# Performance work log

Hardware: AMD Instinct MI355X
Metric: run time of the kernel (lower is better)

Reference implementation:

```python
import jax, jax.numpy as jnp
import numpy as np

N, F, T, E, TS, H = 10000, 64, 8, 160000, 200, 128
K = max(1, int(N * 0.5))
EPS = 1e-8


def layer_norm(x, g, b):
    m = x.mean(-1, keepdims=True)
    v = ((x - m) ** 2).mean(-1, keepdims=True)
    return (x - m) * jax.lax.rsqrt(v + 1e-5) * g + b


def setup_inputs() -> dict:
    key = jax.random.key(0)
    ks = jax.random.split(key, 16)
    s = lambda i, shape, scale=0.05: jax.random.normal(ks[i], shape, jnp.float32) * scale
    return {
        "x_seq": jax.random.normal(ks[0], (T, N, F), jnp.float32),
        "h0": jnp.zeros((N, H), jnp.float32),
        "c0": jnp.zeros((N, H), jnp.float32),
        "time_series": jax.random.normal(ks[1], (TS, N), jnp.float32),
        "Wx": s(2, (4, H, F)),            # gate order: input, forget, output, modulation
        "bx": jnp.zeros((4, H), jnp.float32),
        "Wh": s(3, (4, H, H)),
        "bh": jnp.zeros((4, H), jnp.float32),
        "ln_mod_g": jnp.ones((H,), jnp.float32),
        "ln_mod_b": jnp.zeros((H,), jnp.float32),
        "map_W": s(4, (3, H, H)),         # p1_i0, p2_i0, p2_i1
        "pool_vec": jax.random.normal(ks[5], (H, 1), jnp.float32),
        "lstm_Wih": s(6, (4 * H, N), 0.01),
        "lstm_Whh": s(7, (4 * H, H)),
        "lstm_bih": jnp.zeros((4 * H,), jnp.float32),
        "lstm_bhh": jnp.zeros((4 * H,), jnp.float32),
        "mlp_W1": s(8, (H, 2 * H)),
        "mlp_b1": jnp.zeros((H,), jnp.float32),
        "mlp_ln_g": jnp.ones((H,), jnp.float32),
        "mlp_ln_b": jnp.zeros((H,), jnp.float32),
        "mlp_W2": s(9, (H // 2, H)),
        "mlp_b2": jnp.zeros((H // 2,), jnp.float32),
        "mlp_W3": s(10, (1, H // 2)),
        "mlp_b3": jnp.zeros((1,), jnp.float32),
        "edge_index": jax.random.randint(ks[11], (2, E), 0, N, jnp.int32),
    }


def _forward(x_seq, h0, c0, time_series, Wx, bx, Wh, bh, ln_mod_g, ln_mod_b,
             map_W, pool_vec, lstm_Wih, lstm_Whh, lstm_bih, lstm_bhh,
             mlp_W1, mlp_b1, mlp_ln_g, mlp_ln_b, mlp_W2, mlp_b2, mlp_W3, mlp_b3,
             edge_index):
    src, dst = edge_index[0], edge_index[1]
    # GCN symmetric norm with self-loops: D^{-1/2}(A+I)D^{-1/2}
    deg = 1.0 + jax.ops.segment_sum(jnp.ones((E,), jnp.float32), dst, num_segments=N)
    dis = jax.lax.rsqrt(deg)
    enorm = dis[src] * dis[dst]
    self_norm = dis * dis

    def aggregate(hfeat):  # one shared gather/scatter for all 4 gates, [N, 4H]
        out = jax.ops.segment_sum(hfeat[src] * enorm[:, None], dst, num_segments=N)
        return out + hfeat * self_norm[:, None]

    bias = (bx + bh).reshape(4 * H)

    def cell(x, h, c):
        lin = (jnp.einsum('nf,ghf->ngh', x, Wx).reshape(N, 4 * H)
               + jnp.einsum('nd,ghd->ngh', h, Wh).reshape(N, 4 * H))
        pre = (aggregate(lin) + bias).reshape(N, 4, H)  # aggregation is linear -> fuse x- and h-branches
        i = jax.nn.relu(pre[:, 0])
        f = jax.nn.relu(pre[:, 1])
        o = jax.nn.relu(pre[:, 2])
        g = jnp.tanh(layer_norm(pre[:, 3], ln_mod_g, ln_mod_b))
        c_new = f * c + i * g
        return o * jnp.tanh(c_new), c_new

    # jump_connection_parallel over strides p in {1, 2}
    last = []
    for p in (1, 2):
        for off in range(p):
            h, c = h0, c0
            for t in range(off, T, p):
                h, c = cell(x_seq[t], h, c)
            last.append(h)
    hidden = sum(last[j] @ map_W[j].T for j in range(3))  # p1_i0 + p2_i0 + p2_i1

    # DGPool
    v = pool_vec / (jnp.linalg.norm(pool_vec) + EPS)
    sc = (hidden @ v).squeeze(-1)
    sc = (sc - sc.mean()) / (sc.std() + EPS)
    sig = jax.nn.sigmoid(sc)
    x_scaled = hidden * sig[:, None]
    _, idx = jax.lax.top_k(sig, K)
    new_x = x_scaled[idx]
    ss = -jnp.sort(-sig)
    pool_loss = -(jnp.log(ss[:K] + EPS).sum() + jnp.log(1.0 - ss[K:] + EPS).sum()) / N
    high = new_x.mean(axis=0)

    # raw time-series LSTM (torch gate order i, f, g, o)
    def step(carry, x_t):
        hh, cc = carry
        z = lstm_Wih @ x_t + lstm_bih + lstm_Whh @ hh + lstm_bhh
        i_, f_, g_, o_ = jnp.split(z, 4)
        cc = jax.nn.sigmoid(f_) * cc + jax.nn.sigmoid(i_) * jnp.tanh(g_)
        return (jax.nn.sigmoid(o_) * jnp.tanh(cc), cc), None

    (h_last, _), _ = jax.lax.scan(step, (jnp.zeros(H, jnp.float32), jnp.zeros(H, jnp.float32)), time_series)

    fusion = jnp.concatenate([high, h_last])
    m = jax.nn.relu(mlp_W1 @ fusion + mlp_b1)
    m = layer_norm(m, mlp_ln_g, mlp_ln_b)      # dropout = identity (eval mode)
    m = jax.nn.relu(mlp_W2 @ m + mlp_b2)
    pred = mlp_W3 @ m + mlp_b3
    return pred, pool_loss


def reference(x_seq, h0, c0, time_series, Wx, bx, Wh, bh, ln_mod_g, ln_mod_b,
              map_W, pool_vec, lstm_Wih, lstm_Whh, lstm_bih, lstm_bhh,
              mlp_W1, mlp_b1, mlp_ln_g, mlp_ln_b, mlp_W2, mlp_b2, mlp_W3, mlp_b3,
              edge_index):
    return _forward(x_seq, h0, c0, time_series, Wx, bx, Wh, bh, ln_mod_g, ln_mod_b,
                    map_W, pool_vec, lstm_Wih, lstm_Whh, lstm_bih, lstm_bhh,
                    mlp_W1, mlp_b1, mlp_ln_g, mlp_ln_b, mlp_W2, mlp_b2, mlp_W3, mlp_b3,
                    edge_index)
```

## Files before the change

kernel.cpp:

```cpp
#include <hip/hip_runtime.h>
#include <hip/hip_bf16.h>
#include <math.h>

#define NN 10000
#define FF 64
#define TSTEPS 8
#define EE 160000
#define TSS 200
#define HH 128
#define KK 5000
#define G4 512
#define KIN 192
#define EPSF 1e-8f

typedef __attribute__((ext_vector_type(8))) short short8v;
typedef __attribute__((ext_vector_type(4))) float f32x4;

__device__ inline float wred(float v){
  #pragma unroll
  for (int off = 32; off > 0; off >>= 1) v += __shfl_xor(v, off);
  return v;
}

__device__ inline unsigned short f2b(float f) {
  union { __hip_bfloat16 h; unsigned short u; } cv;
  cv.h = __float2bfloat16(f);
  return cv.u;
}
__device__ inline float b2f(unsigned short u) {
  return __uint_as_float(((unsigned int)u) << 16);
}


__global__ void k_setup_w(const float* Wx, const float* Wh, const float* bx, const float* bh,
                          const float* mapW, unsigned short* Wfrag, float* biasC, float* mapWr) {
  int idx = blockIdx.x * 256 + threadIdx.x;
  {
    int jj = idx & 7, l = (idx >> 3) & 63, ntg = (idx >> 9) & 31, ks = idx >> 14;
    int k = ks * 32 + ((l >> 4) << 3) + jj;
    int gh = ntg * 16 + (l & 15);
    int g = gh >> 7, hh = gh & 127;
    float v = (k < FF) ? Wx[(g * HH + hh) * FF + k] : Wh[(g * HH + hh) * HH + (k - FF)];
    Wfrag[idx] = f2b(v);
  }
  if (idx < G4) biasC[idx] = bx[idx] + bh[idx];
  if (idx < 3 * HH * HH) {
    int s = idx / (HH * HH), r = idx % (HH * HH);
    int d = r / HH, j = r % HH;
    mapWr[idx] = mapW[(s * HH + j) * HH + d];
  }
}

__global__ void k_zero(int* deg, int* cursor, int* rank, float* acc, float* high) {
  int i = blockIdx.x * 256 + threadIdx.x;
  if (i < NN) { deg[i] = 0; cursor[i] = 0; rank[i] = 0; }
  if (i < 16) acc[i] = 0.f;
  if (i < 128) high[i] = 0.f;
}

__global__ void k_deg(const int* ei, int* deg) {
  int e = blockIdx.x * 256 + threadIdx.x;
  if (e < EE) atomicAdd(&deg[ei[EE + e]], 1);
}

__global__ void k_norm(const int* deg, float* dis, float* self_norm) {
  int n = blockIdx.x * 256 + threadIdx.x;
  if (n < NN) {
    float d = 1.0f + (float)deg[n];
    dis[n] = rsqrtf(d);
    self_norm[n] = 1.0f / d;
  }
}

__global__ void k_scan(const int* deg, int* row_ptr, int n) {
  __shared__ int buf[1024];
  __shared__ int carry;
  if (threadIdx.x == 0) carry = 0;
  __syncthreads();
  for (int base = 0; base < n; base += 1024) {
    int i = base + threadIdx.x;
    int v = (i < n) ? deg[i] : 0;
    buf[threadIdx.x] = v;
    __syncthreads();
    for (int off = 1; off < 1024; off <<= 1) {
      int t = (threadIdx.x >= off) ? buf[threadIdx.x - off] : 0;
      __syncthreads();
      buf[threadIdx.x] += t;
      __syncthreads();
    }
    if (i < n) row_ptr[i] = carry + buf[threadIdx.x] - v;
    __syncthreads();
    if (threadIdx.x == 1023) carry += buf[1023];
    __syncthreads();
  }
  if (threadIdx.x == 0) row_ptr[n] = carry;
}

__global__ void k_fill(const int* ei, const int* row_ptr, int* cursor, const float* dis,
                       int* col_src, float* col_w) {
  int e = blockIdx.x * 256 + threadIdx.x;
  if (e < EE) {
    int s = ei[e], d = ei[EE + e];
    int pos = row_ptr[d] + atomicAdd(&cursor[d], 1);
    col_src[pos] = s;
    col_w[pos] = dis[s] * dis[d];
  }
}

__global__ void k_init3(const float* h0, const float* c0, unsigned short* hAll, float* cAll) {
  int i = blockIdx.x * 256 + threadIdx.x;
  if (i < NN * HH) {
    unsigned short h = f2b(h0[i]);
    float c = c0[i];
    hAll[i] = h; hAll[NN * HH + i] = h; hAll[2 * NN * HH + i] = h;
    cAll[i] = c; cAll[NN * HH + i] = c; cAll[2 * NN * HH + i] = c;
  }
}

__global__ void k_xcast(const float* x, unsigned short* xb) {
  int i = blockIdx.x * 256 + threadIdx.x;
  float4 v = *(const float4*)(x + (size_t)i * 4);
  ushort4 u;
  u.x = f2b(v.x); u.y = f2b(v.y); u.z = f2b(v.z); u.w = f2b(v.w);
  *(ushort4*)(xb + (size_t)i * 4) = u;
}


__global__ void __launch_bounds__(256) k_aggx8(const unsigned short* xb, const int* row_ptr,
    const int* col_src, const float* col_w, const float* self_n, unsigned short* aggX) {
  __shared__ int es[4][64];
  __shared__ float ew[4][64];
  int wv = threadIdx.x >> 6, lane = threadIdx.x & 63;
  int p = blockIdx.x * 4 + wv;
  int t = p / NN, n = p - t * NN;
  int e0 = row_ptr[n], e1 = row_ptr[n + 1];
  float acc = 0.f;
  for (int eb = e0; eb < e1; eb += 64) {
    int cnt = min(64, e1 - eb);
    if (lane < cnt) { es[wv][lane] = col_src[eb + lane]; ew[wv][lane] = col_w[eb + lane]; }
    __builtin_amdgcn_wave_barrier();
    for (int i = 0; i < cnt; i++)
      acc += b2f(xb[((size_t)t * NN + es[wv][i]) * FF + lane]) * ew[wv][i];
    __builtin_amdgcn_wave_barrier();
  }
  acc += b2f(xb[((size_t)t * NN + n) * FF + lane]) * self_n[n];
  aggX[(size_t)p * FF + lane] = f2b(acc);
}

__global__ void __launch_bounds__(256) k_aggh(const unsigned short* hAll, const int* row_ptr,
    const int* col_src, const float* col_w, const float* self_n, unsigned short* aggH, int M) {
  __shared__ int es[4][64];
  __shared__ float ew[4][64];
  int w = threadIdx.x >> 6, lane = threadIdx.x & 63;
  int m = blockIdx.x * 2 + (w >> 1);
  if (m >= M) return;
  int ch = (w & 1) * 64 + lane;
  int c = (m >= 2 * NN) ? 2 : (m >= NN ? 1 : 0);
  int n = m - c * NN;
  int e0 = row_ptr[n], e1 = row_ptr[n + 1];
  const unsigned short* hb = hAll + (size_t)c * NN * HH;
  float acc = 0.f;
  for (int eb = e0; eb < e1; eb += 64) {
    int cnt = min(64, e1 - eb);
    if (lane < cnt) { es[w][lane] = col_src[eb + lane]; ew[w][lane] = col_w[eb + lane]; }
    __builtin_amdgcn_wave_barrier();
    for (int i = 0; i < cnt; i++)
      acc += b2f(hb[(size_t)es[w][i] * HH + ch]) * ew[w][i];
    __builtin_amdgcn_wave_barrier();
  }
  acc += b2f(hAll[(size_t)m * HH + ch]) * self_n[n];
  aggH[(size_t)m * HH + ch] = f2b(acc);
}

__global__ void __launch_bounds__(512) k_premm(const unsigned short* aggX,
    const unsigned short* aggH, const unsigned short* Wfrag, const float* biasC,
    unsigned short* preB, int M, int r) {
  __shared__ unsigned short Af[1536 * 8];
  int m0 = blockIdx.x * 64;
  int n0 = blockIdx.y * 256;
  int tid = threadIdx.x;
  int l = tid & 63, wid = tid >> 6;
  int wm = wid >> 2, wn = wid & 3;
  #pragma unroll
  for (int q = 0; q < 3; q++) {
    int chunk = tid + q * 512;
    int mt = chunk / 384, rem = chunk - mt * 384;
    int ks = rem >> 6, cl = rem & 63;
    int row = m0 + mt * 16 + (cl & 15);
    int kk = ks * 32 + ((cl >> 4) << 3);
    short8v v = {};
    if (row < M) {
      const unsigned short* src;
      if (kk < FF) {
        int ch = (row >= 2 * NN) ? 2 : (row >= NN ? 1 : 0);
        int n = row - ch * NN;
        int t = (ch == 0) ? r : (2 * r + ch - 1);
        src = aggX + ((size_t)t * NN + n) * FF + kk;
      } else {
        src = aggH + (size_t)row * HH + (kk - FF);
      }
      v = *(const short8v*)src;
    }
    *(short8v*)&Af[chunk * 8] = v;
  }
  __syncthreads();
  f32x4 acc[2][4];
  #pragma unroll
  for (int i = 0; i < 2; i++)
    #pragma unroll
    for (int j = 0; j < 4; j++) acc[i][j] = (f32x4){0.f, 0.f, 0.f, 0.f};
  #pragma unroll
  for (int ks = 0; ks < 6; ks++) {
    short8v a0 = *(const short8v*)&Af[(((wm * 2 + 0) * 6 + ks) * 64 + l) * 8];
    short8v a1 = *(const short8v*)&Af[(((wm * 2 + 1) * 6 + ks) * 64 + l) * 8];
    #pragma unroll
    for (int j = 0; j < 4; j++) {
      int ntg = (n0 >> 4) + wn * 4 + j;
      short8v b = *(const short8v*)(Wfrag + (((size_t)ks * 32 + ntg) * 64 + l) * 8);
      acc[0][j] = __builtin_amdgcn_mfma_f32_16x16x32_bf16(a0, b, acc[0][j], 0, 0, 0);
      acc[1][j] = __builtin_amdgcn_mfma_f32_16x16x32_bf16(a1, b, acc[1][j], 0, 0, 0);
    }
  }
  #pragma unroll
  for (int i = 0; i < 2; i++)
    #pragma unroll
    for (int j = 0; j < 4; j++) {
      int colg = n0 + wn * 64 + j * 16 + (l & 15);
      float bv = biasC[colg];
      #pragma unroll
      for (int rg = 0; rg < 4; rg++) {
        int row = m0 + wm * 32 + i * 16 + ((l >> 4) * 4) + rg;
        if (row < M) preB[(size_t)row * G4 + colg] = f2b(acc[i][j][rg] + bv);
      }
    }
}

__global__ void __launch_bounds__(128) k_gates(const unsigned short* preB, const float* lng,
                                               const float* lnb, unsigned short* h, float* c,
                                               int M) {
  int b = blockIdx.x;
  int j = threadIdx.x;
  const unsigned short* p = preB + (size_t)b * G4;
  float iv = b2f(p[j]), fv = b2f(p[128 + j]), ov = b2f(p[256 + j]), gv = b2f(p[384 + j]);
  float s = wred(gv), s2 = wred(gv * gv);
  __shared__ float sh[4];
  int wid = j >> 6;
  if ((j & 63) == 0) { sh[wid] = s; sh[2 + wid] = s2; }
  __syncthreads();
  float mean = (sh[0] + sh[1]) * (1.f / 128.f);
  float var = (sh[2] + sh[3]) * (1.f / 128.f) - mean * mean;
  float gn = (gv - mean) * rsqrtf(var + 1e-5f) * lng[j] + lnb[j];
  float gt = tanhf(gn);
  float ii = fmaxf(iv, 0.f), ff = fmaxf(fv, 0.f), oo = fmaxf(ov, 0.f);
  size_t ci = (size_t)b * HH + j;
  float cn = ff * c[ci] + ii * gt;
  c[ci] = cn;
  h[ci] = f2b(oo * tanhf(cn));
}

__global__ void __launch_bounds__(256) k_hidden(const unsigned short* hA, const unsigned short* hB,
                                                const unsigned short* hC, const float* Wr,
                                                float* out) {
  __shared__ __align__(16) float As[8][128];
  __shared__ __align__(16) float Bs[8][64];
  int m0 = blockIdx.x * 128, n0 = blockIdx.y * 64;
  int tid = threadIdx.x;
  int tx = tid & 15, ty = tid >> 4;
  float acc[8][4] = {};
  for (int kc = 0; kc < 48; kc++) {
    int k0 = kc * 8;
    const unsigned short* S = (k0 < 128) ? hA : (k0 < 256 ? hB : hC);
    int koff = k0 & 127;
    {
      int ml = tid >> 1, kq = (tid & 1) * 4;
      int m = m0 + ml;
      float4 v = make_float4(0.f, 0.f, 0.f, 0.f);
      if (m < NN) {
        ushort4 u = *(const ushort4*)(S + (size_t)m * HH + koff + kq);
        v.x = b2f(u.x); v.y = b2f(u.y); v.z = b2f(u.z); v.w = b2f(u.w);
      }
      As[kq + 0][ml] = v.x; As[kq + 1][ml] = v.y; As[kq + 2][ml] = v.z; As[kq + 3][ml] = v.w;
    }
    #pragma unroll
    for (int q = 0; q < 2; q++) {
      int e = tid + q * 256;
      int kl = e >> 6, nl = e & 63;
      Bs[kl][nl] = Wr[(size_t)(k0 + kl) * HH + n0 + nl];
    }
    __syncthreads();
    #pragma unroll
    for (int k = 0; k < 8; k++) {
      float4 a0 = *(const float4*)&As[k][ty * 4];
      float4 a1 = *(const float4*)&As[k][64 + ty * 4];
      float4 b0 = *(const float4*)&Bs[k][tx * 4];
      const float av0[4] = {a0.x, a0.y, a0.z, a0.w};
      const float av1[4] = {a1.x, a1.y, a1.z, a1.w};
      const float bv[4] = {b0.x, b0.y, b0.z, b0.w};
      #pragma unroll
      for (int i = 0; i < 4; i++)
        #pragma unroll
        for (int j = 0; j < 4; j++) {
          acc[i][j] += av0[i] * bv[j];
          acc[4 + i][j] += av1[i] * bv[j];
        }
    }
    __syncthreads();
  }
  #pragma unroll
  for (int g = 0; g < 2; g++)
    #pragma unroll
    for (int i = 0; i < 4; i++) {
      int m = m0 + g * 64 + ty * 4 + i;
      if (m < NN) {
        float4 r;
        r.x = acc[g * 4 + i][0]; r.y = acc[g * 4 + i][1];
        r.z = acc[g * 4 + i][2]; r.w = acc[g * 4 + i][3];
        *(float4*)(out + (size_t)m * HH + n0 + tx * 4) = r;
      }
    }
}


__global__ void k_vnorm(const float* pv, float* acc) {
  int t = threadIdx.x;
  float v = pv[t];
  float s = wred(v * v);
  __shared__ float sh[2];
  if ((t & 63) == 0) sh[t >> 6] = s;
  __syncthreads();
  if (t == 0) acc[0] = 1.0f / (sqrtf(sh[0] + sh[1]) + EPSF);
}

__global__ void __launch_bounds__(256) k_sc(const float* hidden, const float* pv, float* acc,
                                            float* sc) {
  int wid = threadIdx.x >> 6, lane = threadIdx.x & 63;
  float2 vv = *(const float2*)(pv + lane * 2);
  float inv = acc[0];
  float ls = 0.f, ls2 = 0.f;
  for (int n = blockIdx.x * 4 + wid; n < NN; n += gridDim.x * 4) {
    float2 hv = *(const float2*)(hidden + (size_t)n * HH + lane * 2);
    float dot = hv.x * vv.x + hv.y * vv.y;
    dot = wred(dot);
    if (lane == 0) {
      float s = dot * inv;
      sc[n] = s;
      ls += s;
      ls2 += s * s;
    }
  }
  __shared__ float sh[8];
  if (lane == 0) { sh[wid] = ls; sh[4 + wid] = ls2; }
  __syncthreads();
  if (threadIdx.x == 0) {
    atomicAdd(&acc[1], sh[0] + sh[1] + sh[2] + sh[3]);
    atomicAdd(&acc[2], sh[4] + sh[5] + sh[6] + sh[7]);
  }
}

__global__ void k_sig(const float* sc, const float* acc, float* sig) {
  int n = blockIdx.x * 256 + threadIdx.x;
  if (n < NN) {
    float mean = acc[1] * (1.f / NN);
    float var = acc[2] * (1.f / NN) - mean * mean;
    float sd = sqrtf(fmaxf(var, 0.f)) + EPSF;
    float z = (sc[n] - mean) / sd;
    sig[n] = 1.f / (1.f + expf(-z));
  }
}

__global__ void __launch_bounds__(256) k_rank(const float* sc, int* rank) {
  __shared__ float sj[1024];
  int i = blockIdx.x * 256 + threadIdx.x;
  int j0 = blockIdx.y * 1024;
  for (int k = threadIdx.x; k < 1024; k += 256) {
    int j = j0 + k;
    sj[k] = (j < NN) ? sc[j] : -3.0e38f;
  }
  __syncthreads();
  float si = (i < NN) ? sc[i] : 0.f;
  int jmax = NN - j0; if (jmax > 1024) jmax = 1024;
  int cnt = 0;
  for (int k = 0; k < jmax; k++) {
    float v = sj[k];
    int j = j0 + k;
    cnt += (v > si) || (v == si && j < i);
  }
  if (i < NN && cnt) atomicAdd(&rank[i], cnt);
}

__global__ void __launch_bounds__(256) k_plogs(const float* sig, const int* rank, float* acc) {
  int i = blockIdx.x * 256 + threadIdx.x;
  float v = 0.f;
  if (i < NN) {
    float s = sig[i];
    v = (rank[i] < KK) ? logf(s + EPSF) : logf(1.f - s + EPSF);
  }
  v = wred(v);
  __shared__ float sh[4];
  if ((threadIdx.x & 63) == 0) sh[threadIdx.x >> 6] = v;
  __syncthreads();
  if (threadIdx.x == 0) atomicAdd(&acc[3], sh[0] + sh[1] + sh[2] + sh[3]);
}

__global__ void __launch_bounds__(128) k_high(const float* hidden, const float* sig,
                                              const int* rank, float* high) {
  int ch = threadIdx.x;
  int n0 = blockIdx.x * 128;
  float a = 0.f;
  for (int q = 0; q < 128; q++) {
    int n = n0 + q;
    if (n >= NN) break;
    if (rank[n] < KK) a += hidden[(size_t)n * HH + ch] * sig[n];
  }
  atomicAdd(&high[ch], a);
}


__global__ void __launch_bounds__(256) k_zpre2(const float* Wih, const float* ts, float* part) {
  __shared__ __align__(16) float As[16][64];
  __shared__ __align__(16) float Bs[16][64];
  int m0 = blockIdx.x * 64;
  int n0 = blockIdx.y * 64;
  int ks = blockIdx.z;
  int kbeg = ks * 624;
  int kend = (ks == 15) ? NN : kbeg + 624;
  int tid = threadIdx.x;
  int tx = tid & 15, ty = tid >> 4;
  int lm = tid >> 2, kq = (tid & 3) * 4;
  bool bvalid = (n0 + lm) < TSS;
  float acc[4][4] = {};
  for (int k0 = kbeg; k0 < kend; k0 += 16) {
    {
      float4 v = *(const float4*)(Wih + (size_t)(m0 + lm) * NN + k0 + kq);
      As[kq + 0][lm] = v.x; As[kq + 1][lm] = v.y; As[kq + 2][lm] = v.z; As[kq + 3][lm] = v.w;
    }
    {
      float4 v = make_float4(0.f, 0.f, 0.f, 0.f);
      if (bvalid) v = *(const float4*)(ts + (size_t)(n0 + lm) * NN + k0 + kq);
      Bs[kq + 0][lm] = v.x; Bs[kq + 1][lm] = v.y; Bs[kq + 2][lm] = v.z; Bs[kq + 3][lm] = v.w;
    }
    __syncthreads();
    #pragma unroll
    for (int k = 0; k < 16; k++) {
      float4 a0 = *(const float4*)&As[k][ty * 4];
      float4 b0 = *(const float4*)&Bs[k][tx * 4];
      const float av[4] = {a0.x, a0.y, a0.z, a0.w};
      const float bv[4] = {b0.x, b0.y, b0.z, b0.w};
      #pragma unroll
      for (int i = 0; i < 4; i++)
        #pragma unroll
        for (int j = 0; j < 4; j++)
          acc[i][j] += av[i] * bv[j];
    }
    __syncthreads();
  }
  float* pd = part + ((size_t)ks << 17);
  #pragma unroll
  for (int i = 0; i < 4; i++) {
    float4 r4 = make_float4(acc[i][0], acc[i][1], acc[i][2], acc[i][3]);
    *(float4*)(pd + (size_t)(m0 + ty * 4 + i) * 256 + n0 + tx * 4) = r4;
  }
}

__global__ void __launch_bounds__(256) k_zred(const float* part, float* zpre) {
  int r = blockIdx.x;
  int t = threadIdx.x;
  int base = r * 256 + t;
  float s = 0.f;
  #pragma unroll
  for (int k = 0; k < 16; k++) s += part[(k << 17) + base];
  if (t < TSS) zpre[(size_t)t * G4 + r] = s;
}

__global__ void __attribute__((amdgpu_waves_per_eu(1, 2))) __launch_bounds__(512)
k_lstm(const float* Whh, const float* bih, const float* bhh,
       const float* zpre, float* h_last) {
  __shared__ float gI[128], gF[128], gG[128], gO[128];
  int tid = threadIdx.x;
  int w = tid >> 6, l = tid & 63;
  int gate = w >> 1;
  int colbase = (w & 1) * 64;
  float wreg[128];
  #pragma unroll
  for (int q = 0; q < 32; q++) {
    float4 v = *(const float4*)(Whh + (size_t)tid * HH + 4 * q);
    wreg[4 * q + 0] = v.x; wreg[4 * q + 1] = v.y;
    wreg[4 * q + 2] = v.z; wreg[4 * q + 3] = v.w;
  }
  float bias = bih[tid] + bhh[tid];
  float h2a = 0.f, h2b = 0.f;
  float cc0 = 0.f, cc1 = 0.f;
  for (int t = 0; t < TSS; t++) {
    float d = bias + zpre[(size_t)t * G4 + tid];
    #pragma unroll
    for (int k = 0; k < 128; k += 2) {
      float ha = __uint_as_float(__builtin_amdgcn_readlane(__float_as_uint(h2a), k >> 1));
      float hb = __uint_as_float(__builtin_amdgcn_readlane(__float_as_uint(h2b), k >> 1));
      d += wreg[k] * ha + wreg[k + 1] * hb;
    }
    float a = (gate == 2) ? tanhf(d) : (1.f / (1.f + expf(-d)));
    if (gate == 0) gI[colbase + l] = a;
    else if (gate == 1) gF[colbase + l] = a;
    else if (gate == 2) gG[colbase + l] = a;
    else gO[colbase + l] = a;
    __syncthreads();
    float2 iv = *(const float2*)&gI[2 * l];
    float2 fv = *(const float2*)&gF[2 * l];
    float2 gv = *(const float2*)&gG[2 * l];
    float2 ov = *(const float2*)&gO[2 * l];
    cc0 = fv.x * cc0 + iv.x * gv.x;
    cc1 = fv.y * cc1 + iv.y * gv.y;
    h2a = ov.x * tanhf(cc0);
    h2b = ov.y * tanhf(cc1);
    __syncthreads();
  }
  if (tid < 64) { h_last[2 * tid] = h2a; h_last[2 * tid + 1] = h2b; }
}


__global__ void __launch_bounds__(256) k_mlp(const float* high, const float* hlast, const float* acc,
    const float* W1, const float* b1, const float* lng, const float* lnb,
    const float* W2, const float* b2, const float* W3, const float* b3, float* out) {
  __shared__ float fus[256];
  __shared__ float m1[128];
  __shared__ float m2[64];
  __shared__ float red[4];
  int t = threadIdx.x;
  fus[t] = (t < 128) ? high[t] * (1.f / KK) : hlast[t - 128];
  __syncthreads();
  if (t < 128) {
    float a = b1[t];
    for (int k = 0; k < 256; k++) a += W1[t * 256 + k] * fus[k];
    m1[t] = fmaxf(a, 0.f);
  }
  __syncthreads();
  if (t < 128) {
    float x = m1[t];
    float s = wred(x), s2 = wred(x * x);
    if ((t & 63) == 0) { red[t >> 6] = s; red[2 + (t >> 6)] = s2; }
  }
  __syncthreads();
  if (t < 128) {
    float mean = (red[0] + red[1]) * (1.f / 128.f);
    float var = (red[2] + red[3]) * (1.f / 128.f) - mean * mean;
    float xn = (m1[t] - mean) * rsqrtf(var + 1e-5f) * lng[t] + lnb[t];
    __syncthreads();
    m1[t] = xn;
  } else {
    __syncthreads();
  }
  __syncthreads();
  if (t < 64) {
    float a = b2[t];
    for (int k = 0; k < 128; k++) a += W2[t * 128 + k] * m1[k];
    m2[t] = fmaxf(a, 0.f);
  }
  __syncthreads();
  if (t < 64) {
    float a = W3[t] * m2[t];
    a = wred(a);
    if (t == 0) {
      out[0] = a + b3[0];
      out[1] = -acc[3] * (1.f / NN);
    }
  }
}


extern "C" void kernel_launch(void* const* d_in, const int* in_sizes, int n_in,
                              void* d_out, int out_size, void* d_ws, size_t ws_size,
                              hipStream_t stream) {
  const float* x_seq = (const float*)d_in[0];
  const float* h0    = (const float*)d_in[1];
  const float* c0    = (const float*)d_in[2];
  const float* ts    = (const float*)d_in[3];
  const float* Wx    = (const float*)d_in[4];
  const float* bx    = (const float*)d_in[5];
  const float* Wh    = (const float*)d_in[6];
  const float* bh    = (const float*)d_in[7];
  const float* lng   = (const float*)d_in[8];
  const float* lnb   = (const float*)d_in[9];
  const float* mapW  = (const float*)d_in[10];
  const float* pv    = (const float*)d_in[11];
  const float* Wih   = (const float*)d_in[12];
  const float* Whh   = (const float*)d_in[13];
  const float* bih   = (const float*)d_in[14];
  const float* bhh   = (const float*)d_in[15];
  const float* W1    = (const float*)d_in[16];
  const float* b1    = (const float*)d_in[17];
  const float* mlng  = (const float*)d_in[18];
  const float* mlnb  = (const float*)d_in[19];
  const float* W2    = (const float*)d_in[20];
  const float* b2    = (const float*)d_in[21];
  const float* W3    = (const float*)d_in[22];
  const float* b3    = (const float*)d_in[23];
  const int*   ei    = (const int*)d_in[24];

  char* wsp = (char*)d_ws;
  size_t off = 0;
  auto carve = [&](size_t bytes) -> char* {
    char* p = wsp + off;
    off += (bytes + 255) & ~(size_t)255;
    return p;
  };
  unsigned short* Wfrag = (unsigned short*)carve(98304 * 2);
  float* biasC   = (float*)carve(G4 * 4);
  float* mapWr   = (float*)carve(3 * HH * HH * 4);
  int*   degi    = (int*)carve(NN * 4);
  int*   cursor  = (int*)carve(NN * 4);
  int*   rankb   = (int*)carve(NN * 4);
  int*   row_ptr = (int*)carve((NN + 1) * 4);
  float* dis     = (float*)carve(NN * 4);
  float* self_n  = (float*)carve(NN * 4);
  int*   col_src = (int*)carve(EE * 4);
  float* col_w   = (float*)carve(EE * 4);
  unsigned short* hAll = (unsigned short*)carve((size_t)3 * NN * HH * 2);
  float*          cAll = (float*)carve((size_t)3 * NN * HH * 4);
  unsigned short* x2b  = (unsigned short*)carve((size_t)TSTEPS * NN * FF * 2);
  unsigned short* aggX = (unsigned short*)carve((size_t)TSTEPS * NN * FF * 2);
  unsigned short* aggH = (unsigned short*)carve((size_t)3 * NN * HH * 2);
  unsigned short* preB = (unsigned short*)carve((size_t)3 * NN * G4 * 2);
  float* hidden  = (float*)carve((size_t)NN * HH * 4);
  float* sc      = (float*)carve(NN * 4);
  float* sig     = (float*)carve(NN * 4);
  float* acc     = (float*)carve(16 * 4);
  float* high    = (float*)carve(128 * 4);
  float* zpre    = (float*)carve((size_t)TSS * G4 * 4);
  float* hlast   = (float*)carve(128 * 4);

  k_setup_w<<<384, 256, 0, stream>>>(Wx, Wh, bx, bh, mapW, Wfrag, biasC, mapWr);
  k_zero<<<40, 256, 0, stream>>>(degi, cursor, rankb, acc, high);
  k_deg<<<625, 256, 0, stream>>>(ei, degi);
  k_norm<<<40, 256, 0, stream>>>(degi, dis, self_n);
  k_scan<<<1, 1024, 0, stream>>>(degi, row_ptr, NN);
  k_fill<<<625, 256, 0, stream>>>(ei, row_ptr, cursor, dis, col_src, col_w);
  k_init3<<<5000, 256, 0, stream>>>(h0, c0, hAll, cAll);
  k_xcast<<<5000, 256, 0, stream>>>(x_seq, x2b);

  k_aggx8<<<20000, 256, 0, stream>>>(x2b, row_ptr, col_src, col_w, self_n, aggX);

  for (int r = 0; r < TSTEPS; r++) {
    int M = (r < 4) ? 3 * NN : NN;
    k_aggh<<<M / 2, 256, 0, stream>>>(hAll, row_ptr, col_src, col_w, self_n, aggH, M);
    k_premm<<<dim3((M + 63) / 64, 2), 512, 0, stream>>>(aggX, aggH, Wfrag, biasC, preB, M, r);
    k_gates<<<M, 128, 0, stream>>>(preB, lng, lnb, hAll, cAll, M);
  }

  k_hidden<<<dim3(79, 2), 256, 0, stream>>>(hAll, hAll + (size_t)NN * HH,
                                            hAll + (size_t)2 * NN * HH, mapWr, hidden);
  k_vnorm<<<1, 128, 0, stream>>>(pv, acc);
  k_sc<<<250, 256, 0, stream>>>(hidden, pv, acc, sc);
  k_sig<<<40, 256, 0, stream>>>(sc, acc, sig);
  k_rank<<<dim3(40, 10), 256, 0, stream>>>(sc, rankb);
  k_plogs<<<40, 256, 0, stream>>>(sig, rankb, acc);
  k_high<<<79, 128, 0, stream>>>(hidden, sig, rankb, high);

  k_zpre2<<<dim3(8, 4, 16), 256, 0, stream>>>(Wih, ts, (float*)preB);
  k_zred<<<512, 256, 0, stream>>>((float*)preB, zpre);
  k_lstm<<<1, 512, 0, stream>>>(Whh, bih, bhh, zpre, hlast);

  k_mlp<<<1, 256, 0, stream>>>(high, hlast, acc, W1, b1, mlng, mlnb, W2, b2, W3, b3,
                               (float*)d_out);
}
```

Baseline: 1.219 ms.

## Split LSTM recurrent matvec across 1024 threads with K-halved partial sums

The single-block sequential LSTM kernel now uses 1024 threads. Each gate row's 128-long recurrent dot product is split into two halves of 64, held in registers by separate thread groups, and the two partial sums are combined through shared memory. This halves the serial dependency chain and register footprint per thread on the 200-step critical path, and the redundant cell-state update is simplified. In exchange it adds an extra shared-memory round trip, leaves only half the threads doing activations, and keeps two barriers per step at a larger block size.

```diff
diff --git a/kernel.cpp b/kernel.cpp
--- a/kernel.cpp
+++ b/kernel.cpp
@@ -472,49 +472,45 @@
   if (t < TSS) zpre[(size_t)t * G4 + r] = s;
 }
 
-__global__ void __attribute__((amdgpu_waves_per_eu(1, 2))) __launch_bounds__(512)
-k_lstm(const float* Whh, const float* bih, const float* bhh,
-       const float* zpre, float* h_last) {
-  __shared__ float gI[128], gF[128], gG[128], gO[128];
+__global__ void __launch_bounds__(1024) k_lstm(const float* Whh, const float* bih, const float* bhh,
+                                               const float* zpre, float* h_last) {
+  __shared__ float part[2][512];
+  __shared__ float gact[512];
   int tid = threadIdx.x;
+  int half = tid >> 9;
+  int r = tid & 511;
   int w = tid >> 6, l = tid & 63;
-  int gate = w >> 1;
-  int colbase = (w & 1) * 64;
-  float wreg[128];
-  #pragma unroll
-  for (int q = 0; q < 32; q++) {
-    float4 v = *(const float4*)(Whh + (size_t)tid * HH + 4 * q);
-    wreg[4 * q + 0] = v.x; wreg[4 * q + 1] = v.y;
-    wreg[4 * q + 2] = v.z; wreg[4 * q + 3] = v.w;
-  }
-  float bias = bih[tid] + bhh[tid];
-  float h2a = 0.f, h2b = 0.f;
-  float cc0 = 0.f, cc1 = 0.f;
+  float w64[64];
+  #pragma unroll
+  for (int q = 0; q < 16; q++) {
+    float4 v = *(const float4*)(Whh + (size_t)r * HH + 64 * half + 4 * q);
+    w64[4 * q + 0] = v.x; w64[4 * q + 1] = v.y;
+    w64[4 * q + 2] = v.z; w64[4 * q + 3] = v.w;
+  }
+  float bias = bih[r] + bhh[r];
+  int jbase = (w >= 8) ? 64 : 0;
+  float hreg = 0.f, creg = 0.f;
   for (int t = 0; t < TSS; t++) {
-    float d = bias + zpre[(size_t)t * G4 + tid];
-    #pragma unroll
-    for (int k = 0; k < 128; k += 2) {
-      float ha = __uint_as_float(__builtin_amdgcn_readlane(__float_as_uint(h2a), k >> 1));
-      float hb = __uint_as_float(__builtin_amdgcn_readlane(__float_as_uint(h2b), k >> 1));
-      d += wreg[k] * ha + wreg[k + 1] * hb;
-    }
-    float a = (gate == 2) ? tanhf(d) : (1.f / (1.f + expf(-d)));
-    if (gate == 0) gI[colbase + l] = a;
-    else if (gate == 1) gF[colbase + l] = a;
-    else if (gate == 2) gG[colbase + l] = a;
-    else gO[colbase + l] = a;
-    __syncthreads();
-    float2 iv = *(const float2*)&gI[2 * l];
-    float2 fv = *(const float2*)&gF[2 * l];
-    float2 gv = *(const float2*)&gG[2 * l];
-    float2 ov = *(const float2*)&gO[2 * l];
-    cc0 = fv.x * cc0 + iv.x * gv.x;
-    cc1 = fv.y * cc1 + iv.y * gv.y;
-    h2a = ov.x * tanhf(cc0);
-    h2b = ov.y * tanhf(cc1);
-    __syncthreads();
-  }
-  if (tid < 64) { h_last[2 * tid] = h2a; h_last[2 * tid + 1] = h2b; }
+    float d = 0.f;
+    #pragma unroll
+    for (int j = 0; j < 64; j++) {
+      float hj = __uint_as_float(__builtin_amdgcn_readlane(__float_as_uint(hreg), j));
+      d += w64[j] * hj;
+    }
+    part[half][r] = d;
+    __syncthreads();
+    if (tid < 512) {
+      float dd = part[0][r] + part[1][r] + bias + zpre[(size_t)t * G4 + r];
+      float a = ((r >> 7) == 2) ? tanhf(dd) : (1.f / (1.f + expf(-dd)));
+      gact[r] = a;
+    }
+    __syncthreads();
+    int j = jbase + l;
+    creg = gact[128 + j] * creg + gact[j] * gact[256 + j];
+    hreg = gact[384 + j] * tanhf(creg);
+  }
+  if (w == 0) h_last[l] = hreg;
+  else if (w == 8) h_last[64 + l] = hreg;
 }
 
 
@@ -657,7 +653,7 @@
 
   k_zpre2<<<dim3(8, 4, 16), 256, 0, stream>>>(Wih, ts, (float*)preB);
   k_zred<<<512, 256, 0, stream>>>((float*)preB, zpre);
-  k_lstm<<<1, 512, 0, stream>>>(Whh, bih, bhh, zpre, hlast);
+  k_lstm<<<1, 1024, 0, stream>>>(Whh, bih, bhh, zpre, hlast);
 
   k_mlp<<<1, 256, 0, stream>>>(high, hlast, acc, W1, b1, mlng, mlnb, W2, b2, W3, b3,
                                (float*)d_out);
```

New measurement: 1.177 ms. 3.5% less time.
